# Kernel tuning notes

Hardware: AMD Instinct MI355X
Metric: run time of the kernel (lower is better)

## Reference

```python
import jax, jax.numpy as jnp
import numpy as np

WS = 7       # window_size
SS = 3       # shift_size
HEADS = 6
HD = 32      # head_dim
DIM = 192    # embedding_dim
MLP_RATIO = 4
SCALE = HD ** -0.5
MM = WS * WS
NEG = -1e9


def _rel_index():
    # Swin relative-position index, shape [MM, MM], values in [0, (2*WS-1)^2)
    coords = np.stack(np.meshgrid(np.arange(WS), np.arange(WS), indexing='ij')).reshape(2, -1)
    rel = coords[:, :, None] - coords[:, None, :]          # [2, MM, MM]
    rel = rel.transpose(1, 2, 0).astype(np.int64)          # [MM, MM, 2]
    rel[:, :, 0] += WS - 1
    rel[:, :, 1] += WS - 1
    rel[:, :, 0] *= 2 * WS - 1
    return rel.sum(-1)                                     # [MM, MM]


def _shift_mask(h, w):
    # attention mask for shifted windows, shape [nh*nw, MM, MM]
    img = np.zeros((h, w), dtype=np.float32)
    cnt = 0
    for hs in (slice(0, -WS), slice(-WS, -SS), slice(-SS, None)):
        for ws_ in (slice(0, -WS), slice(-WS, -SS), slice(-SS, None)):
            img[hs, ws_] = cnt
            cnt += 1
    mw = img.reshape(h // WS, WS, w // WS, WS).transpose(0, 2, 1, 3).reshape(-1, MM)
    diff = mw[:, None, :] - mw[:, :, None]
    return np.where(diff != 0, NEG, 0.0).astype(np.float32)


def _ln(x, g, b):
    m = x.mean(-1, keepdims=True)
    v = ((x - m) ** 2).mean(-1, keepdims=True)
    return (x - m) / jnp.sqrt(v + 1e-5) * g + b


def setup_inputs() -> dict:
    key = jax.random.key(0)
    ks = jax.random.split(key, 8)
    inner = HEADS * HD

    def n(k, shape, s=0.02):
        return jax.random.normal(k, shape, jnp.float32) * s

    return {
        'x': jax.random.normal(ks[0], (64, DIM, 56, 56), jnp.float32),
        'ln1_g': jnp.ones((DIM,), jnp.float32),
        'ln1_b': jnp.zeros((DIM,), jnp.float32),
        'qkv_w': n(ks[1], (3 * inner, DIM)),
        'out_w': n(ks[2], (DIM, inner)),
        'out_b': jnp.zeros((DIM,), jnp.float32),
        'ln2_g': jnp.ones((DIM,), jnp.float32),
        'ln2_b': jnp.zeros((DIM,), jnp.float32),
        'mlp_w1': n(ks[3], (MLP_RATIO * DIM, DIM)),
        'mlp_b1': jnp.zeros((MLP_RATIO * DIM,), jnp.float32),
        'mlp_w2': n(ks[4], (DIM, MLP_RATIO * DIM)),
        'mlp_b2': jnp.zeros((DIM,), jnp.float32),
        'rel_table': n(ks[5], ((2 * WS - 1) ** 2, HEADS)),
    }


def reference(x, ln1_g, ln1_b, qkv_w, out_w, out_b, ln2_g, ln2_b,
              mlp_w1, mlp_b1, mlp_w2, mlp_b2, rel_table):
    b, c, h, w = x.shape
    nh, nw = h // WS, w // WS

    # cyclic shift
    xs = jnp.roll(x, (-SS, -SS), axis=(2, 3))
    # window partition: [b,c,h,w] -> [b*nh*nw, MM, c]
    xw = (xs.reshape(b, c, nh, WS, nw, WS)
            .transpose(0, 2, 4, 3, 5, 1)
            .reshape(b * nh * nw, MM, c))

    # --- attention (PreNorm) ---
    y = _ln(xw, ln1_g, ln1_b)
    qkv = y @ qkv_w.T                                 # [Bw, MM, 3*inner]
    q, k, v = jnp.split(qkv, 3, axis=-1)

    def to_heads(t):
        return t.reshape(-1, MM, HEADS, HD).transpose(0, 2, 1, 3)  # [Bw,H,MM,HD]

    q, k, v = to_heads(q), to_heads(k), to_heads(v)
    logits = jnp.einsum('bhid,bhjd->bhij', q, k) * SCALE           # [Bw,H,MM,MM]

    idx = jnp.asarray(_rel_index())
    bias = rel_table[idx.reshape(-1)].reshape(MM, MM, HEADS).transpose(2, 0, 1)  # [H,MM,MM]
    smask = jnp.asarray(_shift_mask(h, w))                         # [nh*nw,MM,MM]

    logits = (logits.reshape(b, nh * nw, HEADS, MM, MM)
              + bias[None, None] + smask[None, :, None])
    attn = jax.nn.softmax(logits, axis=-1).reshape(b * nh * nw, HEADS, MM, MM)
    o = jnp.einsum('bhij,bhjd->bhid', attn, v)                     # [Bw,H,MM,HD]
    o = o.transpose(0, 2, 1, 3).reshape(-1, MM, HEADS * HD)
    xw = xw + o @ out_w.T + out_b

    # --- MLP (PreNorm) ---
    y = _ln(xw, ln2_g, ln2_b)
    xw = xw + jax.nn.gelu(y @ mlp_w1.T + mlp_b1, approximate=False) @ mlp_w2.T + mlp_b2

    # window reverse + reverse shift
    xr = (xw.reshape(b, nh, nw, WS, WS, c)
            .transpose(0, 5, 1, 3, 2, 4)
            .reshape(b, c, h, w))
    return jnp.roll(xr, (SS, SS), axis=(2, 3))
```

## Files before the change

### kernel.cpp

```cpp
#include <hip/hip_runtime.h>
#include <hip/hip_bf16.h>
#include <hip/hip_fp8.h>

typedef unsigned short u16;
typedef unsigned int u32;
typedef unsigned char u8;
typedef __attribute__((ext_vector_type(4))) float fx4;
typedef __attribute__((ext_vector_type(8))) __bf16 bf8;

#define NEGV -1e9f
#define LOG2E 1.4426950408889634f
#define SCALE2 (0.17677669529663687f*1.4426950408889634f)

static __device__ __forceinline__ u16 f2bu(float f){
    __hip_bfloat16 h = __float2bfloat16(f);
    return *reinterpret_cast<u16*>(&h);
}
static __device__ __forceinline__ float b2f(u16 u){
    __hip_bfloat16 h;
    *reinterpret_cast<u16*>(&h) = u;
    return __bfloat162float(h);
}
static __device__ __forceinline__ u8 f2f8(float v){
    __hip_fp8_e4m3 t(v);
    return *reinterpret_cast<u8*>(&t);
}
static __device__ __forceinline__ float gelu_f(float v){
    const float z = v*0.70710678118654752f;
    const float x = fabsf(z);
    const float t = 1.f/(1.f + 0.3275911f*x);
    const float p = t*(0.254829592f + t*(-0.284496736f + t*(1.421413741f
                   + t*(-1.453152027f + t*1.061405429f))));
    float er = 1.f - p*__builtin_amdgcn_exp2f(-x*x*LOG2E);
    er = (z < 0.f) ? -er : er;
    return 0.5f*v*(1.f + er);
}

__global__ __launch_bounds__(256) void f2b4_kernel(
        const float* __restrict__ s0, const float* __restrict__ s1,
        const float* __restrict__ s2, const float* __restrict__ s3,
        u16* __restrict__ d0, u16* __restrict__ d1,
        u16* __restrict__ d2, u8* __restrict__ d3){
    int i = blockIdx.x*256 + threadIdx.x;
    if (i < 110592) d0[i] = f2bu(s0[i]);
    if (i < 36864)  d1[i] = f2bu(s1[i]);
    if (i < 147456){ d2[i] = f2bu(s2[i]); d3[i] = f2f8(s3[i]*16.f); }
}

__global__ __launch_bounds__(256) void ltab_kernel(const float* __restrict__ rel_table,
                                                   float* __restrict__ LT){
    const int blk = blockIdx.x;
    const int cls = blk/6, h = blk - cls*6;
    float* T = LT + blk*4096;
    for (int e = threadIdx.x; e < 4096; e += 256){
        const int i = e>>6, j = e&63;
        float v = NEGV;
        if (i < 49 && j < 49){
            const int id = i/7, im = i-id*7, jd = j/7, jm = j-jd*7;
            const int ridx = (id-jd+6)*13 + (im-jm+6);
            const float bias = rel_table[ridx*6 + h];
            const int ri = (cls&2) ? (id<4?1:2) : 0;
            const int rj = (cls&2) ? (jd<4?1:2) : 0;
            const int ci = (cls&1) ? (im<4?1:2) : 0;
            const int cj = (cls&1) ? (jm<4?1:2) : 0;
            v = bias + ((ri==rj && ci==cj) ? 0.f : NEGV);
        }
        T[e] = v * LOG2E;
    }
}

__global__ __launch_bounds__(256) void partition_ln_kernel(
        const float* __restrict__ x, const float* __restrict__ g, const float* __restrict__ bta,
        u16* __restrict__ xw, u16* __restrict__ y){
    __shared__ float lds[192*57];
    const int bi = blockIdx.x;
    const int b = bi/56, i = bi%56;
    const int si = (i+3)%56;
    const float* src = x + (size_t)b*602112 + (size_t)si*56;
    for (int e = threadIdx.x; e < 10752; e += 256){
        int c = e/56, j = e%56;
        lds[c*57 + j] = src[(size_t)c*3136 + j];
    }
    __syncthreads();
    const int wrow_base = (b*8 + i/7)*8;
    const int prow = (i%7)*7;
    for (int e = threadIdx.x; e < 10752; e += 256){
        int j = e/192, c = e%192;
        int t = (wrow_base + j/7)*49 + prow + (j%7);
        xw[(size_t)t*192 + c] = f2bu(lds[c*57 + (j+3)%56]);
    }
    const int wv = threadIdx.x>>6, l = threadIdx.x&63;
    for (int j = wv; j < 56; j += 4){
        const int jj = (j+3)%56;
        float v0 = lds[l*57 + jj], v1 = lds[(l+64)*57 + jj], v2 = lds[(l+128)*57 + jj];
        float s = v0+v1+v2;
        #pragma unroll
        for (int o=32;o;o>>=1) s += __shfl_xor(s, o, 64);
        const float mean = s*(1.f/192.f);
        float d0 = v0-mean, d1 = v1-mean, d2 = v2-mean;
        float qv = d0*d0 + d1*d1 + d2*d2;
        #pragma unroll
        for (int o=32;o;o>>=1) qv += __shfl_xor(qv, o, 64);
        const float rstd = rsqrtf(qv*(1.f/192.f) + 1e-5f);
        const int t = (wrow_base + j/7)*49 + prow + (j%7);
        u16* yr = y + (size_t)t*192;
        yr[l]     = f2bu(d0*rstd*g[l]     + bta[l]);
        yr[l+64]  = f2bu(d1*rstd*g[l+64]  + bta[l+64]);
        yr[l+128] = f2bu(d2*rstd*g[l+128] + bta[l+128]);
    }
}

__global__ __launch_bounds__(256) void reverse_kernel(const u16* __restrict__ xw, float* __restrict__ out){
    __shared__ float lds[192*57];
    const int bi = blockIdx.x;
    const int b = bi/56, h = bi%56;
    const int i = (h+53)%56;
    const int wrow_base = (b*8 + i/7)*8;
    const int prow = (i%7)*7;
    for (int e = threadIdx.x; e < 10752; e += 256){
        int j = e/192, c = e%192;
        int t = (wrow_base + j/7)*49 + prow + (j%7);
        lds[c*57 + j] = b2f(xw[(size_t)t*192 + c]);
    }
    __syncthreads();
    float* dst = out + (size_t)b*602112 + (size_t)h*56;
    for (int e = threadIdx.x; e < 10752; e += 256){
        int c = e/56, w = e%56;
        dst[(size_t)c*3136 + w] = lds[c*57 + (w+53)%56];
    }
}

template<int ROWS>
static __device__ __forceinline__ void stage_tile(const char* __restrict__ g, size_t row0,
                                                  int kc, int pitch, u16* ldsbase, int tid){
    const int w = tid>>6, lane = tid&63;
    const int sub = lane>>3;
    const int b16 = (lane&7) ^ sub;
    #pragma unroll
    for (int i=0; i<ROWS/32; ++i){
        const int row = i*32 + w*8 + sub;
        const char* src = g + (row0+row)*(size_t)pitch + (size_t)kc*128 + b16*16;
        u16* dst = ldsbase + i*2048 + w*512;
#if __has_builtin(__builtin_amdgcn_global_load_lds)
        __builtin_amdgcn_global_load_lds(
            (const __attribute__((address_space(1))) u32*)src,
            (__attribute__((address_space(3))) u32*)dst, 16, 0, 0);
#else
        *(uint4*)(dst + lane*8) = *(const uint4*)src;
#endif
    }
}

static __device__ __forceinline__ bf8 rd_frag16(const u16* lds, int row, int boff){
    const char* p = (const char*)lds + row*128 + (boff ^ ((row&7)<<4));
    return *(const bf8*)p;
}
static __device__ __forceinline__ long rd_frag8(const u16* lds, int row, int boff){
    const char* p = (const char*)lds + row*128 + (boff ^ ((row&7)<<4));
    return *(const long*)p;
}

template<int KEL,int ESZ,int ACT,int RES,int LNOUT,int OUT,int HASB>
__global__ __launch_bounds__(256,2) void gemm_kernel(
    const void* __restrict__ Av, const void* __restrict__ Bv,
    const float* __restrict__ bias, const u16* __restrict__ res,
    void* __restrict__ out,
    const float* __restrict__ lng, const float* __restrict__ lnb,
    u16* __restrict__ yout, int Ntot, float ascale)
{
    constexpr int NKT = (KEL*ESZ)/128;
    constexpr int KKS = (ESZ==1)?4:2;
    constexpr int PITCH = KEL*ESZ;
    __shared__ __align__(16) u16 lds[40960];
    const int tid = threadIdx.x;
    const int wv = tid>>6, l = tid&63, lr = l&15, lg = l>>4;
    const int wm = wv&1, wn = wv>>1;
    const size_t row0 = (size_t)blockIdx.x*128;
    const int n0 = blockIdx.y*192;
    const char* A = (const char*)Av;
    const char* Bblk = (const char*)Bv + (size_t)n0*PITCH;

    stage_tile<128>(A, row0, 0, PITCH, lds, tid);
    stage_tile<192>(Bblk, 0, 0, PITCH, lds+16384, tid);
    __syncthreads();

    fx4 acc[4][6] = {};
    for (int kc=0; kc<NKT; ++kc){
        const int cur = kc & 1;
        u16* Ac = cur ? (u16*)lds+8192  : (u16*)lds;
        u16* Bc = cur ? (u16*)lds+28672 : (u16*)lds+16384;
        if (kc+1 < NKT){
            u16* An = cur ? (u16*)lds       : (u16*)lds+8192;
            u16* Bn = cur ? (u16*)lds+16384 : (u16*)lds+28672;
            stage_tile<128>(A, row0, kc+1, PITCH, An, tid);
            stage_tile<192>(Bblk, 0, kc+1, PITCH, Bn, tid);
        }
        #pragma unroll
        for (int kk=0; kk<KKS; ++kk){
            if constexpr (ESZ==2){
                bf8 af[4], bfr[6];
                #pragma unroll
                for (int r=0;r<4;r++) af[r]  = rd_frag16(Ac, wm*64 + r*16 + lr, kk*64 + lg*16);
                #pragma unroll
                for (int c=0;c<6;c++) bfr[c] = rd_frag16(Bc, wn*96 + c*16 + lr, kk*64 + lg*16);
                #pragma unroll
                for (int r=0;r<4;r++)
                    #pragma unroll
                    for (int c=0;c<6;c++)
                        acc[r][c] = __builtin_amdgcn_mfma_f32_16x16x32_bf16(af[r], bfr[c], acc[r][c], 0,0,0);
            } else {
                long af[4], bfr[6];
                #pragma unroll
                for (int r=0;r<4;r++) af[r]  = rd_frag8(Ac, wm*64 + r*16 + lr, kk*32 + lg*8);
                #pragma unroll
                for (int c=0;c<6;c++) bfr[c] = rd_frag8(Bc, wn*96 + c*16 + lr, kk*32 + lg*8);
                #pragma unroll
                for (int r=0;r<4;r++)
                    #pragma unroll
                    for (int c=0;c<6;c++)
                        acc[r][c] = __builtin_amdgcn_mfma_f32_16x16x32_fp8_fp8(af[r], bfr[c], acc[r][c], 0,0,0);
            }
        }
        __syncthreads();
    }

    #pragma unroll
    for (int r=0;r<4;r++)
        #pragma unroll
        for (int c=0;c<6;c++){
            const int col = n0 + wn*96 + c*16 + lr;
            const float bv = HASB ? bias[col] : 0.f;
            #pragma unroll
            for (int q=0;q<4;q++){
                const size_t grow = row0 + wm*64 + r*16 + lg*4 + q;
                float v = fmaf(acc[r][c][q], ascale, bv);
                if (ACT) v = gelu_f(v);
                if (RES) v += b2f(res[grow*Ntot + col]);
                acc[r][c][q] = v;
                if (OUT==1) ((u16*)out)[grow*Ntot + col] = f2bu(v);
                else        ((u8*)out)[grow*(size_t)Ntot + col] = f2f8(v);
            }
        }
    if (LNOUT){
        float* redS = (float*)lds;
        #pragma unroll
        for (int r=0;r<4;r++)
            #pragma unroll
            for (int q=0;q<4;q++){
                float s  = 0.f, s2 = 0.f;
                #pragma unroll
                for (int c=0;c<6;c++){ float v = acc[r][c][q]; s += v; s2 += v*v; }
                #pragma unroll
                for (int o=8;o;o>>=1){ s += __shfl_xor(s, o, 64); s2 += __shfl_xor(s2, o, 64); }
                if (lr == 0){
                    const int rowl = wm*64 + r*16 + lg*4 + q;
                    redS[(wn*128 + rowl)*2 + 0] = s;
                    redS[(wn*128 + rowl)*2 + 1] = s2;
                }
            }
        __syncthreads();
        #pragma unroll
        for (int r=0;r<4;r++)
            #pragma unroll
            for (int q=0;q<4;q++){
                const int rowl = wm*64 + r*16 + lg*4 + q;
                const float S  = redS[rowl*2+0] + redS[(128+rowl)*2+0];
                const float S2 = redS[rowl*2+1] + redS[(128+rowl)*2+1];
                const float mean = S*(1.f/192.f);
                const float rstd = rsqrtf(S2*(1.f/192.f) - mean*mean + 1e-5f);
                const size_t grow = row0 + rowl;
                #pragma unroll
                for (int c=0;c<6;c++){
                    const int col = wn*96 + c*16 + lr;
                    yout[grow*192 + col] = f2bu((acc[r][c][q]-mean)*rstd*lng[col] + lnb[col]);
                }
            }
    }
}

__global__ __launch_bounds__(64) void attn_kernel(const u16* __restrict__ qkv,
                                                  const float* __restrict__ LT,
                                                  u16* __restrict__ o)
{
    __shared__ u16 pa[64*72];
    __shared__ u16 vt[32*72];
    const int bid = blockIdx.x;
    const int widx = bid/6, h = bid - widx*6;
    const int wi = widx & 63;
    const int nhi = wi>>3, nwi = wi&7;
    const int l = threadIdx.x, lr = l&15, lg = l>>4;
    const u16* base = qkv + (size_t)widx*49*576;
    const int cls = ((nhi==7)?2:0) | ((nwi==7)?1:0);
    const float* Th = LT + (size_t)(cls*6 + h)*4096;

    bf8 qf[4], kf[4];
    #pragma unroll
    for (int t=0;t<4;t++){
        const int row = min(t*16 + lr, 48);
        qf[t] = *(const bf8*)(base + (size_t)row*576 + h*32 + lg*8);
        kf[t] = *(const bf8*)(base + (size_t)row*576 + 192 + h*32 + lg*8);
    }
    for (int e=l; e<480; e+=64){
        int d = e/15, j = 49 + (e - d*15);
        vt[d*72 + j] = 0;
    }
    for (int e=l; e<784; e+=64){
        int j = e>>4, dp = e&15;
        u32 val = *(const u32*)(base + (size_t)j*576 + 384 + h*32 + dp*2);
        vt[(dp*2)*72 + j]   = (u16)(val & 0xffffu);
        vt[(dp*2+1)*72 + j] = (u16)(val >> 16);
    }

    fx4 acc[4][4] = {};
    #pragma unroll
    for (int ti=0;ti<4;ti++)
        #pragma unroll
        for (int tj=0;tj<4;tj++)
            acc[ti][tj] = __builtin_amdgcn_mfma_f32_16x16x32_bf16(qf[ti], kf[tj], acc[ti][tj], 0,0,0);

    #pragma unroll
    for (int ti=0;ti<4;ti++){
        #pragma unroll
        for (int reg=0;reg<4;reg++){
            const int i = ti*16 + lg*4 + reg;
            const float* rowp = Th + i*64;
            #pragma unroll
            for (int tj=0;tj<4;tj++)
                acc[ti][tj][reg] = fmaf(acc[ti][tj][reg], SCALE2, rowp[tj*16 + lr]);
        }
    }
    #pragma unroll
    for (int ti=0;ti<4;ti++){
        #pragma unroll
        for (int reg=0;reg<4;reg++){
            float mx = fmaxf(fmaxf(acc[ti][0][reg], acc[ti][1][reg]),
                             fmaxf(acc[ti][2][reg], acc[ti][3][reg]));
            #pragma unroll
            for (int o2=8;o2;o2>>=1) mx = fmaxf(mx, __shfl_xor(mx, o2, 64));
            float sum = 0.f;
            #pragma unroll
            for (int tj=0;tj<4;tj++){
                float p = __builtin_amdgcn_exp2f(acc[ti][tj][reg] - mx);
                acc[ti][tj][reg] = p;
                sum += p;
            }
            #pragma unroll
            for (int o2=8;o2;o2>>=1) sum += __shfl_xor(sum, o2, 64);
            const float rs = 1.f/sum;
            #pragma unroll
            for (int tj=0;tj<4;tj++) acc[ti][tj][reg] *= rs;
        }
    }
    #pragma unroll
    for (int ti=0;ti<4;ti++)
        #pragma unroll
        for (int tj=0;tj<4;tj++)
            #pragma unroll
            for (int reg=0;reg<4;reg++)
                pa[(ti*16 + lg*4 + reg)*72 + tj*16 + lr] = f2bu(acc[ti][tj][reg]);
    __syncthreads();

    fx4 oacc[4][2] = {};
    #pragma unroll
    for (int kk=0;kk<2;kk++){
        bf8 bfr[2];
        #pragma unroll
        for (int cd=0;cd<2;cd++)
            bfr[cd] = *(const bf8*)(vt + (cd*16+lr)*72 + kk*32 + lg*8);
        #pragma unroll
        for (int ti=0;ti<4;ti++){
            bf8 afr = *(const bf8*)(pa + (ti*16+lr)*72 + kk*32 + lg*8);
            #pragma unroll
            for (int cd=0;cd<2;cd++)
                oacc[ti][cd] = __builtin_amdgcn_mfma_f32_16x16x32_bf16(afr, bfr[cd], oacc[ti][cd], 0,0,0);
        }
    }
    u16* ob = o + (size_t)widx*49*192 + h*32;
    #pragma unroll
    for (int ti=0;ti<4;ti++)
        #pragma unroll
        for (int cd=0;cd<2;cd++)
            #pragma unroll
            for (int q=0;q<4;q++){
                const int i = ti*16 + lg*4 + q;
                if (i < 49) ob[(size_t)i*192 + cd*16 + lr] = f2bu(oacc[ti][cd][q]);
            }
}

extern "C" void kernel_launch(void* const* d_in, const int* in_sizes, int n_in,
                              void* d_out, int out_size, void* d_ws, size_t ws_size,
                              hipStream_t stream)
{
    const float* x      = (const float*)d_in[0];
    const float* ln1_g  = (const float*)d_in[1];
    const float* ln1_b  = (const float*)d_in[2];
    const float* qkv_w  = (const float*)d_in[3];
    const float* out_w  = (const float*)d_in[4];
    const float* out_b  = (const float*)d_in[5];
    const float* ln2_g  = (const float*)d_in[6];
    const float* ln2_b  = (const float*)d_in[7];
    const float* mlp_w1 = (const float*)d_in[8];
    const float* mlp_b1 = (const float*)d_in[9];
    const float* mlp_w2 = (const float*)d_in[10];
    const float* mlp_b2 = (const float*)d_in[11];
    const float* rel_t  = (const float*)d_in[12];

    char* ws = (char*)d_ws;
    u16*   Ybuf = (u16*)ws;
    float* LTab = (float*)(ws + 77070336);
    u16*   XWbuf = (u16*)(ws + 154140672);
    u16*   QKVH  = (u16*)(ws + 231211008);
    u8*    Hbuf  = (u8*)(ws + 231211008);
    u16*   Wq = (u16*)(ws + 539492352);
    u16*   Wo = Wq + 110592;
    u16*   W1 = Wo + 36864;
    u8*    W2f8 = (u8*)(W1 + 147456);

    f2b4_kernel<<<576,256,0,stream>>>(qkv_w, out_w, mlp_w1, mlp_w2, Wq, Wo, W1, W2f8);
    ltab_kernel<<<24,256,0,stream>>>(rel_t, LTab);

    partition_ln_kernel<<<3584,256,0,stream>>>(x, ln1_g, ln1_b, XWbuf, Ybuf);
    gemm_kernel<192,2,0,0,0,1,0><<<dim3(1568,3),256,0,stream>>>(Ybuf, Wq, nullptr, nullptr, QKVH,
                                                                nullptr, nullptr, nullptr, 576, 1.f);
    attn_kernel<<<24576,64,0,stream>>>(QKVH, LTab, Ybuf);
    gemm_kernel<192,2,0,1,1,1,1><<<dim3(1568,1),256,0,stream>>>(Ybuf, Wo, out_b, XWbuf, XWbuf,
                                                                ln2_g, ln2_b, Ybuf, 192, 1.f);
    gemm_kernel<192,2,1,0,0,2,1><<<dim3(1568,4),256,0,stream>>>(Ybuf, W1, mlp_b1, nullptr, Hbuf,
                                                                nullptr, nullptr, nullptr, 768, 1.f);
    gemm_kernel<768,1,0,1,0,1,1><<<dim3(1568,1),256,0,stream>>>(Hbuf, W2f8, mlp_b2, XWbuf, Ybuf,
                                                                nullptr, nullptr, nullptr, 192, 0.0625f);
    reverse_kernel<<<3584,256,0,stream>>>(Ybuf, (float*)d_out);
}
```

Baseline: 769.0 us.

## Fold LayerNorm affine into weights and apply normalization in GEMM epilogue

Folds the LayerNorm gamma into the QKV and MLP1 weights, and precomputes per-column weight sums and beta/bias constants. The LN-producing kernels then emit only per-row (mean, rstd) stats instead of writing a normalized bf16 activation tensor. The consuming GEMMs read the raw residual stream and apply rstd*(acc - mean*wsum) + c in the epilogue. This removes the full normalized-activation write and re-read, at the cost of numerics: the GEMM now runs on un-normalized bf16 inputs, and the mean is subtracted after accumulation, which can cancel precision. It also packs the fp8 epilogue conversion.

```diff
diff --git a/kernel.cpp b/kernel.cpp
--- a/kernel.cpp
+++ b/kernel.cpp
@@ -36,15 +36,44 @@
     return 0.5f*v*(1.f + er);
 }
 
-__global__ __launch_bounds__(256) void f2b4_kernel(
-        const float* __restrict__ s0, const float* __restrict__ s1,
-        const float* __restrict__ s2, const float* __restrict__ s3,
-        u16* __restrict__ d0, u16* __restrict__ d1,
-        u16* __restrict__ d2, u8* __restrict__ d3){
+__global__ __launch_bounds__(256) void f2b2_kernel(
+        const float* __restrict__ s1, const float* __restrict__ s3,
+        u16* __restrict__ d1, u8* __restrict__ d3){
     int i = blockIdx.x*256 + threadIdx.x;
-    if (i < 110592) d0[i] = f2bu(s0[i]);
     if (i < 36864)  d1[i] = f2bu(s1[i]);
-    if (i < 147456){ d2[i] = f2bu(s2[i]); d3[i] = f2f8(s3[i]*16.f); }
+    if (i < 147456) d3[i] = f2f8(s3[i]*16.f);
+}
+
+__global__ __launch_bounds__(256) void wprep_kernel(
+        const float* __restrict__ qkv_w, const float* __restrict__ g1, const float* __restrict__ b1,
+        const float* __restrict__ w1,    const float* __restrict__ g2, const float* __restrict__ b2,
+        const float* __restrict__ mb1,
+        u16* __restrict__ WqP, float* __restrict__ wsq, float* __restrict__ ccq,
+        u16* __restrict__ W1P, float* __restrict__ ws1, float* __restrict__ cc1){
+    const int row = blockIdx.x*4 + (threadIdx.x>>6);
+    const int l = threadIdx.x & 63;
+    const int isq = row < 576;
+    const int n = isq ? row : row - 576;
+    if (row >= 1344) return;
+    const float* src = (isq ? qkv_w : w1) + (size_t)n*192;
+    const float* g = isq ? g1 : g2;
+    const float* b = isq ? b1 : b2;
+    u16* dst = (isq ? WqP : W1P) + (size_t)n*192;
+    float sw = 0.f, sc = 0.f;
+    #pragma unroll
+    for (int t=0;t<3;t++){
+        const int k = l + t*64;
+        const float wv = src[k];
+        const float wp = wv*g[k];
+        dst[k] = f2bu(wp);
+        sw += wp; sc += b[k]*wv;
+    }
+    #pragma unroll
+    for (int o=32;o;o>>=1){ sw += __shfl_xor(sw,o,64); sc += __shfl_xor(sc,o,64); }
+    if (!l){
+        if (isq){ wsq[n]=sw; ccq[n]=sc; }
+        else    { ws1[n]=sw; cc1[n]=sc + mb1[n]; }
+    }
 }
 
 __global__ __launch_bounds__(256) void ltab_kernel(const float* __restrict__ rel_table,
@@ -70,8 +99,7 @@
 }
 
 __global__ __launch_bounds__(256) void partition_ln_kernel(
-        const float* __restrict__ x, const float* __restrict__ g, const float* __restrict__ bta,
-        u16* __restrict__ xw, u16* __restrict__ y){
+        const float* __restrict__ x, u16* __restrict__ xw, float2* __restrict__ RS1){
     __shared__ float lds[192*57];
     const int bi = blockIdx.x;
     const int b = bi/56, i = bi%56;
@@ -102,11 +130,10 @@
         #pragma unroll
         for (int o=32;o;o>>=1) qv += __shfl_xor(qv, o, 64);
         const float rstd = rsqrtf(qv*(1.f/192.f) + 1e-5f);
-        const int t = (wrow_base + j/7)*49 + prow + (j%7);
-        u16* yr = y + (size_t)t*192;
-        yr[l]     = f2bu(d0*rstd*g[l]     + bta[l]);
-        yr[l+64]  = f2bu(d1*rstd*g[l+64]  + bta[l+64]);
-        yr[l+128] = f2bu(d2*rstd*g[l+128] + bta[l+128]);
+        if (l == 0){
+            const int t = (wrow_base + j/7)*49 + prow + (j%7);
+            RS1[t] = make_float2(mean, rstd);
+        }
     }
 }
 
@@ -160,13 +187,14 @@
     return *(const long*)p;
 }
 
-template<int KEL,int ESZ,int ACT,int RES,int LNOUT,int OUT,int HASB>
+template<int KEL,int ESZ,int ACT,int RES,int LNF,int STATS,int OUT,int HASB>
 __global__ __launch_bounds__(256,2) void gemm_kernel(
     const void* __restrict__ Av, const void* __restrict__ Bv,
     const float* __restrict__ bias, const u16* __restrict__ res,
     void* __restrict__ out,
-    const float* __restrict__ lng, const float* __restrict__ lnb,
-    u16* __restrict__ yout, int Ntot, float ascale)
+    const float2* __restrict__ RSin, const float* __restrict__ wsum,
+    const float* __restrict__ cc, float2* __restrict__ RSout,
+    int Ntot, float ascale)
 {
     constexpr int NKT = (KEL*ESZ)/128;
     constexpr int KKS = (ESZ==1)?4:2;
@@ -224,32 +252,74 @@
         __syncthreads();
     }
 
-    #pragma unroll
-    for (int r=0;r<4;r++)
-        #pragma unroll
-        for (int c=0;c<6;c++){
-            const int col = n0 + wn*96 + c*16 + lr;
-            const float bv = HASB ? bias[col] : 0.f;
+    float sA[4][4], sB[4][4];
+    if constexpr (LNF){
+        #pragma unroll
+        for (int r=0;r<4;r++)
             #pragma unroll
             for (int q=0;q<4;q++){
-                const size_t grow = row0 + wm*64 + r*16 + lg*4 + q;
-                float v = fmaf(acc[r][c][q], ascale, bv);
-                if (ACT) v = gelu_f(v);
-                if (RES) v += b2f(res[grow*Ntot + col]);
-                acc[r][c][q] = v;
-                if (OUT==1) ((u16*)out)[grow*Ntot + col] = f2bu(v);
-                else        ((u8*)out)[grow*(size_t)Ntot + col] = f2f8(v);
-            }
-        }
-    if (LNOUT){
+                const float2 st = RSin[row0 + wm*64 + r*16 + lg*4 + q];
+                sA[r][q] = st.y;
+                sB[r][q] = -st.x*st.y;
+            }
+    }
+    float ss[4][4], ss2[4][4];
+    if constexpr (STATS){
+        #pragma unroll
+        for (int r=0;r<4;r++)
+            #pragma unroll
+            for (int q=0;q<4;q++){ ss[r][q]=0.f; ss2[r][q]=0.f; }
+    }
+    #pragma unroll
+    for (int c=0;c<6;c++){
+        const int col = n0 + wn*96 + c*16 + lr;
+        float bv = 0.f, wsc = 0.f, ccc = 0.f;
+        if constexpr (HASB) bv = bias[col];
+        if constexpr (LNF){ wsc = wsum[col]; ccc = cc[col]; }
+        #pragma unroll
+        for (int r=0;r<4;r++){
+            const size_t grow0 = row0 + wm*64 + r*16 + lg*4;
+            float vq[4];
+            #pragma unroll
+            for (int q=0;q<4;q++){
+                float v = acc[r][c][q];
+                if constexpr (ESZ==1) v *= ascale;
+                if constexpr (LNF) v = fmaf(v, sA[r][q], fmaf(sB[r][q], wsc, ccc));
+                else v += bv;
+                if constexpr (ACT) v = gelu_f(v);
+                if constexpr (RES) v += b2f(res[(grow0+q)*Ntot + col]);
+                if constexpr (STATS){ ss[r][q] += v; ss2[r][q] += v*v; }
+                vq[q] = v;
+            }
+            if constexpr (OUT==1){
+                #pragma unroll
+                for (int q=0;q<4;q++)
+                    ((u16*)out)[(grow0+q)*Ntot + col] = f2bu(vq[q]);
+            } else {
+                u8* ob = (u8*)out + grow0*(size_t)Ntot + col;
+#if __has_builtin(__builtin_amdgcn_cvt_pk_fp8_f32)
+                const u32 p01 = (u32)__builtin_amdgcn_cvt_pk_fp8_f32(vq[0], vq[1], 0, false);
+                const u32 p23 = (u32)__builtin_amdgcn_cvt_pk_fp8_f32(vq[2], vq[3], 0, false);
+                ob[0] = (u8)p01;        ob += Ntot;
+                ob[0] = (u8)(p01>>8);   ob += Ntot;
+                ob[0] = (u8)p23;        ob += Ntot;
+                ob[0] = (u8)(p23>>8);
+#else
+                ob[0] = f2f8(vq[0]); ob += Ntot;
+                ob[0] = f2f8(vq[1]); ob += Ntot;
+                ob[0] = f2f8(vq[2]); ob += Ntot;
+                ob[0] = f2f8(vq[3]);
+#endif
+            }
+        }
+    }
+    if constexpr (STATS){
         float* redS = (float*)lds;
         #pragma unroll
         for (int r=0;r<4;r++)
             #pragma unroll
             for (int q=0;q<4;q++){
-                float s  = 0.f, s2 = 0.f;
-                #pragma unroll
-                for (int c=0;c<6;c++){ float v = acc[r][c][q]; s += v; s2 += v*v; }
+                float s = ss[r][q], s2 = ss2[r][q];
                 #pragma unroll
                 for (int o=8;o;o>>=1){ s += __shfl_xor(s, o, 64); s2 += __shfl_xor(s2, o, 64); }
                 if (lr == 0){
@@ -259,22 +329,13 @@
                 }
             }
         __syncthreads();
-        #pragma unroll
-        for (int r=0;r<4;r++)
-            #pragma unroll
-            for (int q=0;q<4;q++){
-                const int rowl = wm*64 + r*16 + lg*4 + q;
-                const float S  = redS[rowl*2+0] + redS[(128+rowl)*2+0];
-                const float S2 = redS[rowl*2+1] + redS[(128+rowl)*2+1];
-                const float mean = S*(1.f/192.f);
-                const float rstd = rsqrtf(S2*(1.f/192.f) - mean*mean + 1e-5f);
-                const size_t grow = row0 + rowl;
-                #pragma unroll
-                for (int c=0;c<6;c++){
-                    const int col = wn*96 + c*16 + lr;
-                    yout[grow*192 + col] = f2bu((acc[r][c][q]-mean)*rstd*lng[col] + lnb[col]);
-                }
-            }
+        for (int row = tid; row < 128; row += 256){
+            const float S  = redS[row*2+0] + redS[(128+row)*2+0];
+            const float S2 = redS[row*2+1] + redS[(128+row)*2+1];
+            const float mean = S*(1.f/192.f);
+            const float rstd = rsqrtf(S2*(1.f/192.f) - mean*mean + 1e-5f);
+            RSout[row0 + row] = make_float2(mean, rstd);
+        }
     }
 }
 
@@ -406,28 +467,36 @@
     const float* rel_t  = (const float*)d_in[12];
 
     char* ws = (char*)d_ws;
-    u16*   Ybuf = (u16*)ws;
-    float* LTab = (float*)(ws + 77070336);
-    u16*   XWbuf = (u16*)(ws + 154140672);
-    u16*   QKVH  = (u16*)(ws + 231211008);
-    u8*    Hbuf  = (u8*)(ws + 231211008);
-    u16*   Wq = (u16*)(ws + 539492352);
-    u16*   Wo = Wq + 110592;
-    u16*   W1 = Wo + 36864;
-    u8*    W2f8 = (u8*)(W1 + 147456);
-
-    f2b4_kernel<<<576,256,0,stream>>>(qkv_w, out_w, mlp_w1, mlp_w2, Wq, Wo, W1, W2f8);
+    u16*    Ybuf  = (u16*)ws;
+    float*  LTab  = (float*)(ws + 77070336);
+    float2* RS1   = (float2*)(ws + 77600000);
+    float2* RS2   = (float2*)(ws + 79300000);
+    u16*    WqP   = (u16*)(ws + 81000000);
+    float*  wsq   = (float*)(ws + 81300000);
+    float*  ccq   = (float*)(ws + 81310000);
+    u16*    W1P   = (u16*)(ws + 81400000);
+    float*  ws1   = (float*)(ws + 81700000);
+    float*  cc1   = (float*)(ws + 81710000);
+    u16*    XWbuf = (u16*)(ws + 154140672);
+    u16*    QKVH  = (u16*)(ws + 231211008);
+    u8*     Hbuf  = (u8*)(ws + 231211008);
+    u16*    Wo    = (u16*)(ws + 539492352);
+    u8*     W2f8  = (u8*)(ws + 539492352 + 73728);
+
+    f2b2_kernel<<<576,256,0,stream>>>(out_w, mlp_w2, Wo, W2f8);
+    wprep_kernel<<<336,256,0,stream>>>(qkv_w, ln1_g, ln1_b, mlp_w1, ln2_g, ln2_b, mlp_b1,
+                                       WqP, wsq, ccq, W1P, ws1, cc1);
     ltab_kernel<<<24,256,0,stream>>>(rel_t, LTab);
 
-    partition_ln_kernel<<<3584,256,0,stream>>>(x, ln1_g, ln1_b, XWbuf, Ybuf);
-    gemm_kernel<192,2,0,0,0,1,0><<<dim3(1568,3),256,0,stream>>>(Ybuf, Wq, nullptr, nullptr, QKVH,
-                                                                nullptr, nullptr, nullptr, 576, 1.f);
+    partition_ln_kernel<<<3584,256,0,stream>>>(x, XWbuf, RS1);
+    gemm_kernel<192,2,0,0,1,0,1,0><<<dim3(1568,3),256,0,stream>>>(
+        XWbuf, WqP, nullptr, nullptr, QKVH, RS1, wsq, ccq, nullptr, 576, 1.f);
     attn_kernel<<<24576,64,0,stream>>>(QKVH, LTab, Ybuf);
-    gemm_kernel<192,2,0,1,1,1,1><<<dim3(1568,1),256,0,stream>>>(Ybuf, Wo, out_b, XWbuf, XWbuf,
-                                                                ln2_g, ln2_b, Ybuf, 192, 1.f);
-    gemm_kernel<192,2,1,0,0,2,1><<<dim3(1568,4),256,0,stream>>>(Ybuf, W1, mlp_b1, nullptr, Hbuf,
-                                                                nullptr, nullptr, nullptr, 768, 1.f);
-    gemm_kernel<768,1,0,1,0,1,1><<<dim3(1568,1),256,0,stream>>>(Hbuf, W2f8, mlp_b2, XWbuf, Ybuf,
-                                                                nullptr, nullptr, nullptr, 192, 0.0625f);
+    gemm_kernel<192,2,0,1,0,1,1,1><<<dim3(1568,1),256,0,stream>>>(
+        Ybuf, Wo, out_b, XWbuf, XWbuf, nullptr, nullptr, nullptr, RS2, 192, 1.f);
+    gemm_kernel<192,2,1,0,1,0,2,0><<<dim3(1568,4),256,0,stream>>>(
+        XWbuf, W1P, nullptr, nullptr, Hbuf, RS2, ws1, cc1, nullptr, 768, 1.f);
+    gemm_kernel<768,1,0,1,0,0,1,1><<<dim3(1568,1),256,0,stream>>>(
+        Hbuf, W2f8, mlp_b2, XWbuf, Ybuf, nullptr, nullptr, nullptr, nullptr, 192, 0.0625f);
     reverse_kernel<<<3584,256,0,stream>>>(Ybuf, (float*)d_out);
 }
```

After: 795.6 us. +3.5%, slower.
